# Optimization experiments

Hardware: AMD Instinct MI355X
Metric: run time of the kernel (lower is better)

## Reference

```python
import jax, jax.numpy as jnp
import numpy as np

KE = 14.399645351950548  # Coulomb constant e^2/(4 pi eps0) in eV*Angstrom (ASE)
CUTOFF = 10.0
P = 8_000_000    # number of ML-MM pairs
NML = 50_000     # number of ML atoms
NMM = 200_000    # number of MM point charges


def setup_inputs() -> dict:
    key = jax.random.key(0)
    ks = jax.random.split(key, 10)
    return {
        "atomic_charges": jax.random.normal(ks[0], (NML,), dtype=jnp.float32),
        "mm_atomic_charges": jax.random.normal(ks[1], (NMM,), dtype=jnp.float32),
        "atomic_dipoles": jax.random.normal(ks[2], (NML, 3), dtype=jnp.float32),
        "atomic_quadrupoles": jax.random.normal(ks[3], (NML, 3, 3), dtype=jnp.float32),
        "atomic_energies": jax.random.normal(ks[4], (NML,), dtype=jnp.float32),
        # positive distances in [0.5, 12.0) so the cutoff mask is nontrivial
        "mlmm_distances_uv": jax.random.uniform(ks[5], (P,), dtype=jnp.float32, minval=0.5, maxval=12.0),
        "mlmm_vectors_uv": jax.random.normal(ks[6], (P, 3), dtype=jnp.float32),
        "mlmm_outer_product_uv": jax.random.normal(ks[7], (P, 3, 3), dtype=jnp.float32),
        "mlmm_idx_u": jax.random.randint(ks[8], (P,), 0, NML, dtype=jnp.int64),
        "mlmm_idx_v": jax.random.randint(ks[9], (P,), 0, NMM, dtype=jnp.int64),
    }


def reference(atomic_charges, mm_atomic_charges, atomic_dipoles,
              atomic_quadrupoles, atomic_energies,
              mlmm_distances_uv, mlmm_vectors_uv, mlmm_outer_product_uv,
              mlmm_idx_u, mlmm_idx_v):
    d = mlmm_distances_uv                      # [P]
    chi = 1.0 / d                              # [P]
    q_u = atomic_charges[mlmm_idx_u]           # [P] gathered ML charges
    q_v = mm_atomic_charges[mlmm_idx_v]        # [P] gathered MM charges
    Eelec = q_u * q_v * chi                    # charge-charge

    # dipole term
    chi2 = chi * chi
    chi_vectors = mlmm_vectors_uv * chi[:, None]            # r_vec / |r|
    mu_u = atomic_dipoles[mlmm_idx_u]                       # [P,3]
    dot_vu = jnp.sum(chi_vectors * mu_u, axis=1)            # [P]
    Eelec = Eelec - q_v * dot_vu * chi2

    # quadrupole term
    chi3 = chi2 * chi
    Q_u = atomic_quadrupoles[mlmm_idx_u]                    # [P,3,3]
    diag_mean = jnp.trace(mlmm_outer_product_uv, axis1=-2, axis2=-1) / 3.0  # [P]
    eye3 = jnp.eye(3, dtype=mlmm_outer_product_uv.dtype)
    traceless = mlmm_outer_product_uv - diag_mean[:, None, None] * eye3     # [P,3,3]
    chi_traceless = traceless * chi2[:, None, None]         # outer / d^2
    sum_vu = jnp.sum(chi_traceless * Q_u, axis=(1, 2))      # [P]
    Eelec = Eelec + q_v * sum_vu * chi3

    Eelec = KE * Eelec
    Eelec = jnp.where(d <= CUTOFF, Eelec, jnp.zeros_like(Eelec))

    # scatter-add pair energies onto ML atoms
    Eelec_atom = jax.ops.segment_sum(Eelec, mlmm_idx_u, num_segments=NML)
    return atomic_energies + Eelec_atom
```

## Files before the change

### kernel.cpp

```cpp
#include <hip/hip_runtime.h>


static constexpr float KE_F     = 14.399645351950548f;
static constexpr float CUTOFF_F = 10.0f;

typedef float cf4 __attribute__((ext_vector_type(4)));
typedef int   ci4 __attribute__((ext_vector_type(4)));

__global__ void init_out_kernel(const float* __restrict__ energies,
                                float* __restrict__ out, int n) {
    int i = blockIdx.x * blockDim.x + threadIdx.x;
    if (i < n) out[i] = energies[i];
}

__device__ __forceinline__ void pair_contrib(
    float di, int ui, int vi,
    const float* __restrict__ vp,
    const float* __restrict__ op,
    const float* __restrict__ q_ml,
    const float* __restrict__ q_mm,
    const float* __restrict__ mu,
    const float* __restrict__ Q,
    float* __restrict__ out)
{
    if (di > CUTOFF_F) return;
    float chi  = 1.0f / di;
    float chi2 = chi * chi;
    float chi3 = chi2 * chi;
    float chi5 = chi3 * chi2;

    float qu = q_ml[ui];
    float qv = q_mm[vi];

    const float* m = mu + 3 * ui;
    float dot = vp[0]*m[0] + vp[1]*m[1] + vp[2]*m[2];

    const float* qq = Q + 9 * ui;
    float S = op[0]*qq[0] + op[1]*qq[1] + op[2]*qq[2]
            + op[3]*qq[3] + op[4]*qq[4] + op[5]*qq[5]
            + op[6]*qq[6] + op[7]*qq[7] + op[8]*qq[8];
    float dm  = (op[0] + op[4] + op[8]) * (1.0f / 3.0f);
    float trQ = qq[0] + qq[4] + qq[8];

    float E = KE_F * qv * (qu * chi - chi3 * dot + chi5 * (S - dm * trQ));
    unsafeAtomicAdd(out + ui, E);
}

__global__ __launch_bounds__(256) void mlmm_pair_kernel(
    const float* __restrict__ q_ml,
    const float* __restrict__ q_mm,
    const float* __restrict__ mu,
    const float* __restrict__ Q,
    const float* __restrict__ dist,
    const float* __restrict__ vec,
    const float* __restrict__ outer,
    const int*   __restrict__ idx_u,
    const int*   __restrict__ idx_v,
    float* __restrict__ out,
    int n4, int npairs)
{
    int t = blockIdx.x * blockDim.x + threadIdx.x;

    if (t < n4) {
        const cf4* d4  = (const cf4*)dist;
        const ci4* iu4 = (const ci4*)idx_u;
        const ci4* iv4 = (const ci4*)idx_v;
        const cf4* v4  = (const cf4*)vec;
        const cf4* o4  = (const cf4*)outer;

        cf4 d = __builtin_nontemporal_load(d4 + t);
        ci4 u = __builtin_nontemporal_load(iu4 + t);
        ci4 v = __builtin_nontemporal_load(iv4 + t);

        cf4 vv[3];
        #pragma unroll
        for (int k = 0; k < 3; ++k) vv[k] = __builtin_nontemporal_load(v4 + 3 * t + k);
        cf4 oo[9];
        #pragma unroll
        for (int k = 0; k < 9; ++k) oo[k] = __builtin_nontemporal_load(o4 + 9 * t + k);

        const float* vf = (const float*)vv;
        const float* of = (const float*)oo;
        float dd[4] = {d.x, d.y, d.z, d.w};
        int   uu[4] = {u.x, u.y, u.z, u.w};
        int   wv[4] = {v.x, v.y, v.z, v.w};

        #pragma unroll
        for (int p = 0; p < 4; ++p) {
            pair_contrib(dd[p], uu[p], wv[p], vf + 3 * p, of + 9 * p,
                         q_ml, q_mm, mu, Q, out);
        }
    }

    int tail = npairs - 4 * n4;
    if (blockIdx.x == 0 && (int)threadIdx.x < tail) {
        int i = 4 * n4 + threadIdx.x;
        pair_contrib(dist[i], idx_u[i], idx_v[i],
                     vec + 3 * i, outer + 9 * i,
                     q_ml, q_mm, mu, Q, out);
    }
}

extern "C" void kernel_launch(void* const* d_in, const int* in_sizes, int n_in,
                              void* d_out, int out_size, void* d_ws, size_t ws_size,
                              hipStream_t stream) {
    const float* q_ml   = (const float*)d_in[0];
    const float* q_mm   = (const float*)d_in[1];
    const float* mu     = (const float*)d_in[2];
    const float* Q      = (const float*)d_in[3];
    const float* ene    = (const float*)d_in[4];
    const float* dist   = (const float*)d_in[5];
    const float* vec    = (const float*)d_in[6];
    const float* outer  = (const float*)d_in[7];
    const int*   idx_u  = (const int*)d_in[8];
    const int*   idx_v  = (const int*)d_in[9];
    float* out = (float*)d_out;

    int nml    = in_sizes[4];
    int npairs = in_sizes[5];
    int n4     = npairs >> 2;

    {
        int threads = 256;
        int blocks = (nml + threads - 1) / threads;
        init_out_kernel<<<blocks, threads, 0, stream>>>(ene, out, nml);
    }
    {
        int threads = 256;
        int blocks = (n4 + threads - 1) / threads;
        if (blocks < 1) blocks = 1;
        mlmm_pair_kernel<<<blocks, threads, 0, stream>>>(
            q_ml, q_mm, mu, Q, dist, vec, outer, idx_u, idx_v, out, n4, npairs);
    }
}
```

Before: 800.0 us.

## Replace global atomic scatter with LDS-privatized segmented sum over staged pair energies

Splits the work into a pass that writes per-pair energies to workspace, a pass where block groups accumulate energies for a subset of ML atoms in shared memory with LDS atomics, and a final pass that sums per-block partials and adds base energies. This removes millions of random global atomic adds to the output. In exchange it adds workspace traffic: energies are written once and reread, together with idx_u, once per atom subset, and there is a partial buffer. A fallback atomic path runs if the workspace is too small.

```diff
diff --git a/kernel.cpp b/kernel.cpp
--- a/kernel.cpp
+++ b/kernel.cpp
@@ -7,23 +7,21 @@
 typedef float cf4 __attribute__((ext_vector_type(4)));
 typedef int   ci4 __attribute__((ext_vector_type(4)));
 
-__global__ void init_out_kernel(const float* __restrict__ energies,
-                                float* __restrict__ out, int n) {
-    int i = blockIdx.x * blockDim.x + threadIdx.x;
-    if (i < n) out[i] = energies[i];
-}
-
-__device__ __forceinline__ void pair_contrib(
+#define BPG        128
+#define SUBSETS    4
+#define MAX_SUBN   12544
+#define P2_THREADS 1024
+
+__device__ __forceinline__ float pair_energy(
     float di, int ui, int vi,
     const float* __restrict__ vp,
     const float* __restrict__ op,
     const float* __restrict__ q_ml,
     const float* __restrict__ q_mm,
     const float* __restrict__ mu,
-    const float* __restrict__ Q,
-    float* __restrict__ out)
-{
-    if (di > CUTOFF_F) return;
+    const float* __restrict__ Q)
+{
+    if (di > CUTOFF_F) return 0.0f;
     float chi  = 1.0f / di;
     float chi2 = chi * chi;
     float chi3 = chi2 * chi;
@@ -42,11 +40,10 @@
     float dm  = (op[0] + op[4] + op[8]) * (1.0f / 3.0f);
     float trQ = qq[0] + qq[4] + qq[8];
 
-    float E = KE_F * qv * (qu * chi - chi3 * dot + chi5 * (S - dm * trQ));
-    unsafeAtomicAdd(out + ui, E);
-}
-
-__global__ __launch_bounds__(256) void mlmm_pair_kernel(
+    return KE_F * qv * (qu * chi - chi3 * dot + chi5 * (S - dm * trQ));
+}
+
+__global__ __launch_bounds__(256) void pair_energy_kernel(
     const float* __restrict__ q_ml,
     const float* __restrict__ q_mm,
     const float* __restrict__ mu,
@@ -56,7 +53,7 @@
     const float* __restrict__ outer,
     const int*   __restrict__ idx_u,
     const int*   __restrict__ idx_v,
-    float* __restrict__ out,
+    float* __restrict__ E_out,
     int n4, int npairs)
 {
     int t = blockIdx.x * blockDim.x + threadIdx.x;
@@ -69,7 +66,7 @@
         const cf4* o4  = (const cf4*)outer;
 
         cf4 d = __builtin_nontemporal_load(d4 + t);
-        ci4 u = __builtin_nontemporal_load(iu4 + t);
+        ci4 u = iu4[t];
         ci4 v = __builtin_nontemporal_load(iv4 + t);
 
         cf4 vv[3];
@@ -85,20 +82,101 @@
         int   uu[4] = {u.x, u.y, u.z, u.w};
         int   wv[4] = {v.x, v.y, v.z, v.w};
 
+        cf4 e;
         #pragma unroll
         for (int p = 0; p < 4; ++p) {
-            pair_contrib(dd[p], uu[p], wv[p], vf + 3 * p, of + 9 * p,
-                         q_ml, q_mm, mu, Q, out);
+            float ev = pair_energy(dd[p], uu[p], wv[p], vf + 3*p, of + 9*p,
+                                   q_ml, q_mm, mu, Q);
+            ((float*)&e)[p] = ev;
         }
+        ((cf4*)E_out)[t] = e;
     }
 
     int tail = npairs - 4 * n4;
     if (blockIdx.x == 0 && (int)threadIdx.x < tail) {
         int i = 4 * n4 + threadIdx.x;
-        pair_contrib(dist[i], idx_u[i], idx_v[i],
-                     vec + 3 * i, outer + 9 * i,
-                     q_ml, q_mm, mu, Q, out);
-    }
+        E_out[i] = pair_energy(dist[i], idx_u[i], idx_v[i],
+                               vec + 3*i, outer + 9*i, q_ml, q_mm, mu, Q);
+    }
+}
+
+__global__ __launch_bounds__(P2_THREADS) void segsum_lds_kernel(
+    const int*   __restrict__ idx_u,
+    const float* __restrict__ E,
+    float* __restrict__ partial,
+    int n4, int npairs, int subn, int nml)
+{
+    __shared__ float sacc[MAX_SUBN];
+
+    int s  = blockIdx.x >> 7;
+    int b  = blockIdx.x & (BPG - 1);
+    int lo = s * subn;
+    int hi = lo + subn; if (hi > nml) hi = nml;
+
+    for (int j = threadIdx.x; j < subn; j += P2_THREADS) sacc[j] = 0.0f;
+    __syncthreads();
+
+    const ci4* iu4 = (const ci4*)idx_u;
+    const cf4* e4  = (const cf4*)E;
+
+    for (int t = b * P2_THREADS + threadIdx.x; t < n4; t += BPG * P2_THREADS) {
+        ci4 u = iu4[t];
+        cf4 e = e4[t];
+        if (e.x != 0.0f && u.x >= lo && u.x < hi) atomicAdd(&sacc[u.x - lo], e.x);
+        if (e.y != 0.0f && u.y >= lo && u.y < hi) atomicAdd(&sacc[u.y - lo], e.y);
+        if (e.z != 0.0f && u.z >= lo && u.z < hi) atomicAdd(&sacc[u.z - lo], e.z);
+        if (e.w != 0.0f && u.w >= lo && u.w < hi) atomicAdd(&sacc[u.w - lo], e.w);
+    }
+
+    int tail = npairs - 4 * n4;
+    if (b == 0 && (int)threadIdx.x < tail) {
+        int i  = 4 * n4 + threadIdx.x;
+        int ui = idx_u[i];
+        float ev = E[i];
+        if (ev != 0.0f && ui >= lo && ui < hi) atomicAdd(&sacc[ui - lo], ev);
+    }
+
+    __syncthreads();
+    float* dst = partial + (size_t)blockIdx.x * subn;
+    for (int j = threadIdx.x; j < subn; j += P2_THREADS) dst[j] = sacc[j];
+}
+
+__global__ __launch_bounds__(256) void reduce_partials_kernel(
+    const float* __restrict__ energies,
+    const float* __restrict__ partial,
+    float* __restrict__ out,
+    int nml, int subn)
+{
+    int u = blockIdx.x * 256 + threadIdx.x;
+    if (u >= nml) return;
+    int s = u / subn;
+    int j = u - s * subn;
+    const float* p = partial + (size_t)(s * BPG) * subn + j;
+    float acc = energies[u];
+    #pragma unroll 4
+    for (int b = 0; b < BPG; ++b) acc += p[(size_t)b * subn];
+    out[u] = acc;
+}
+
+__global__ void init_out_kernel(const float* __restrict__ energies,
+                                float* __restrict__ out, int n) {
+    int i = blockIdx.x * blockDim.x + threadIdx.x;
+    if (i < n) out[i] = energies[i];
+}
+
+__global__ __launch_bounds__(256) void mlmm_pair_atomic_kernel(
+    const float* __restrict__ q_ml, const float* __restrict__ q_mm,
+    const float* __restrict__ mu,   const float* __restrict__ Q,
+    const float* __restrict__ dist, const float* __restrict__ vec,
+    const float* __restrict__ outer,
+    const int* __restrict__ idx_u,  const int* __restrict__ idx_v,
+    float* __restrict__ out, int npairs)
+{
+    int i = blockIdx.x * blockDim.x + threadIdx.x;
+    if (i >= npairs) return;
+    float ev = pair_energy(dist[i], idx_u[i], idx_v[i],
+                           vec + 3*i, outer + 9*i, q_ml, q_mm, mu, Q);
+    if (ev != 0.0f) unsafeAtomicAdd(out + idx_u[i], ev);
 }
 
 extern "C" void kernel_launch(void* const* d_in, const int* in_sizes, int n_in,
@@ -119,17 +197,35 @@
     int nml    = in_sizes[4];
     int npairs = in_sizes[5];
     int n4     = npairs >> 2;
-
-    {
+    int subn   = (nml + SUBSETS - 1) / SUBSETS;
+
+    size_t e_bytes   = (size_t)npairs * sizeof(float);
+    size_t e_aligned = (e_bytes + 255) & ~(size_t)255;
+    size_t p_bytes   = (size_t)SUBSETS * BPG * subn * sizeof(float);
+    bool   use_fast  = (subn <= MAX_SUBN) && (ws_size >= e_aligned + p_bytes);
+
+    if (use_fast) {
+        float* ws_E = (float*)d_ws;
+        float* ws_P = (float*)((char*)d_ws + e_aligned);
+
+        {
+            int blocks = (n4 + 255) / 256;
+            if (blocks < 1) blocks = 1;
+            pair_energy_kernel<<<blocks, 256, 0, stream>>>(
+                q_ml, q_mm, mu, Q, dist, vec, outer, idx_u, idx_v,
+                ws_E, n4, npairs);
+        }
+        segsum_lds_kernel<<<SUBSETS * BPG, P2_THREADS, 0, stream>>>(
+            idx_u, ws_E, ws_P, n4, npairs, subn, nml);
+        {
+            int blocks = (nml + 255) / 256;
+            reduce_partials_kernel<<<blocks, 256, 0, stream>>>(
+                ene, ws_P, out, nml, subn);
+        }
+    } else {
         int threads = 256;
-        int blocks = (nml + threads - 1) / threads;
-        init_out_kernel<<<blocks, threads, 0, stream>>>(ene, out, nml);
-    }
-    {
-        int threads = 256;
-        int blocks = (n4 + threads - 1) / threads;
-        if (blocks < 1) blocks = 1;
-        mlmm_pair_kernel<<<blocks, threads, 0, stream>>>(
-            q_ml, q_mm, mu, Q, dist, vec, outer, idx_u, idx_v, out, n4, npairs);
-    }
-}
+        init_out_kernel<<<(nml + threads - 1) / threads, threads, 0, stream>>>(ene, out, nml);
+        mlmm_pair_atomic_kernel<<<(npairs + threads - 1) / threads, threads, 0, stream>>>(
+            q_ml, q_mm, mu, Q, dist, vec, outer, idx_u, idx_v, out, npairs);
+    }
+}
```

Result: faster. 718.7 us (-10.2%).
